# Optimization experiments

Measured on AMD Instinct MI355X. Metric: run time of the kernel, lower is better.

The kernel has to match this reference:

```python
import jax, jax.numpy as jnp
import numpy as np

EPS = 1e-3  # BatchNorm eps from module

def _bn(x, g, b, m, v):
    # torch BatchNorm1d (eval): (x - mean) / sqrt(var + eps) * weight + bias
    return (x - m) * (g / jnp.sqrt(v + EPS)) + b

def setup_inputs() -> dict:
    key = jax.random.key(0)
    ks = jax.random.split(key, 16)
    N, Cin, Cout, S = 1_000_000, 16, 64, 20_000
    inputs = jax.random.normal(ks[0], (N, Cin), dtype=jnp.float32)
    unq_inv = jax.random.randint(ks[1], (N,), 0, S, dtype=jnp.int32)

    def bn_params(k, c):
        k1, k2, k3, k4 = jax.random.split(k, 4)
        return (1.0 + 0.01 * jax.random.normal(k1, (c,), jnp.float32),
                0.01 * jax.random.normal(k2, (c,), jnp.float32),
                0.01 * jax.random.normal(k3, (c,), jnp.float32),
                jax.random.uniform(k4, (c,), jnp.float32, 0.5, 1.5))

    W1 = 0.1 * jax.random.normal(ks[2], (Cin, Cout), jnp.float32)
    g1, b1, m1, v1 = bn_params(ks[3], Cout)
    W2a = 0.1 * jax.random.normal(ks[4], (Cin, 2 * Cout), jnp.float32)
    g2a, b2a, m2a, v2a = bn_params(ks[5], 2 * Cout)
    W2b = 0.1 * jax.random.normal(ks[6], (2 * Cout, Cout), jnp.float32)
    g2b, b2b, m2b, v2b = bn_params(ks[7], Cout)

    return dict(inputs=inputs, unq_inv=unq_inv, num_segments=S,
                W1=W1, g1=g1, b1=b1, m1=m1, v1=v1,
                W2a=W2a, g2a=g2a, b2a=b2a, m2a=m2a, v2a=v2a,
                W2b=W2b, g2b=b2b * 0 + g2b, b2b=b2b, m2b=m2b, v2b=v2b)

def reference(inputs, unq_inv, num_segments,
              W1, g1, b1, m1, v1,
              W2a, g2a, b2a, m2a, v2a,
              W2b, g2b, b2b, m2b, v2b):
    # branch 1: Linear -> BN -> ReLU
    x = jax.nn.relu(_bn(inputs @ W1, g1, b1, m1, v1))            # [N, C]
    # branch 2: Linear -> BN -> ReLU -> Linear -> BN -> ReLU
    h = jax.nn.relu(_bn(inputs @ W2a, g2a, b2a, m2a, v2a))       # [N, 2C]
    x2 = jax.nn.relu(_bn(h @ W2b, g2b, b2b, m2b, v2b))           # [N, C]

    # segment reductions over group ids
    x_max = jax.ops.segment_max(x, unq_inv, num_segments=num_segments)  # [S, C]
    x_max = jnp.maximum(x_max, 0.0)  # empty segments -> 0 (x >= 0 post-ReLU)
    group_sum = jax.ops.segment_sum(x, unq_inv, num_segments=num_segments)  # [S, C]
    max_pool = jnp.max(x2, axis=0)                                # [C], global pool
    max_pool = jnp.broadcast_to(max_pool[None, :], x_max.shape)   # [S, C]

    feat = jnp.concatenate((group_sum, x_max, max_pool), axis=1)  # [S, 3C]
    # channel shuffle with groups=3
    S_, C3 = feat.shape
    feat = feat.reshape(S_, 3, C3 // 3).transpose(0, 2, 1).reshape(S_, C3)
    return feat
```

## Files before the change

### kernel.cpp

```cpp
#include <hip/hip_runtime.h>

#define EPS 1e-3f

#define OFF_T2B    7168
#define OFF_MPP    7232
#define OFF_CNT    11328
#define OFF_OFFS   31344
#define OFF_CUR    51360
#define OFF_INPS   71424

typedef short short8 __attribute__((ext_vector_type(8)));
typedef float f32x4 __attribute__((ext_vector_type(4)));

union U4 { unsigned u[4]; short8 s8; };

__device__ inline unsigned short f2bf(float f) {
    unsigned u = __float_as_uint(f);
    return (unsigned short)((u + 0x7FFFu + ((u >> 16) & 1u)) >> 16);
}

__global__ __launch_bounds__(256) void init_k(
    const float* __restrict__ W1,
    const float* __restrict__ g1, const float* __restrict__ b1,
    const float* __restrict__ m1, const float* __restrict__ v1,
    const float* __restrict__ W2a,
    const float* __restrict__ g2a, const float* __restrict__ b2a,
    const float* __restrict__ m2a, const float* __restrict__ v2a,
    const float* __restrict__ W2b,
    const float* __restrict__ g2b, const float* __restrict__ b2b,
    const float* __restrict__ m2b, const float* __restrict__ v2b,
    unsigned short* __restrict__ wsu, float* __restrict__ wsf,
    const int* __restrict__ unq, int* __restrict__ cnt, int N)
{
    const int t = threadIdx.x;
    if (blockIdx.x == 0) {
        for (int i = t; i < 64 * 32; i += 256) {
            int ch = i >> 5, k = i & 31;
            float s = g1[ch] * rsqrtf(v1[ch] + EPS);
            float val = (k < 16) ? W1[k * 64 + ch] * s
                      : (k == 16 ? b1[ch] - m1[ch] * s : 0.f);
            wsu[i] = f2bf(val);
        }
        for (int i = t; i < 128 * 32; i += 256) {
            int ch = i >> 5, k = i & 31;
            float s = g2a[ch] * rsqrtf(v2a[ch] + EPS);
            float val = (k < 16) ? W2a[k * 128 + ch] * s
                      : (k == 16 ? b2a[ch] - m2a[ch] * s : 0.f);
            wsu[2048 + i] = f2bf(val);
        }
        for (int i = t; i < 64 * 128; i += 256) {
            int ch = i >> 7, k = i & 127;
            float s = g2b[ch] * rsqrtf(v2b[ch] + EPS);
            wsu[2048 + 4096 + i] = f2bf(W2b[k * 64 + ch] * s);
        }
        if (t < 64) {
            float s = g2b[t] * rsqrtf(v2b[t] + EPS);
            wsf[OFF_T2B + t] = b2b[t] - m2b[t] * s;
        }
    } else {
        const int i = (blockIdx.x - 1) * 256 + t;
        if (i < N) atomicAdd(&cnt[unq[i]], 1);
    }
}

__global__ __launch_bounds__(1024) void scan_k(
    const int* __restrict__ cnt, int* __restrict__ offs,
    int* __restrict__ cur, int S)
{
    __shared__ int tot[1024];
    const int t = threadIdx.x;
    const int E = (S + 1023) >> 10;
    const int i0 = t * E;
    int run = 0;
    for (int j = 0; j < E; ++j) {
        const int i = i0 + j;
        run += (i < S) ? cnt[i] : 0;
    }
    tot[t] = run;
    __syncthreads();
    for (int d = 1; d < 1024; d <<= 1) {
        int x = (t >= d) ? tot[t - d] : 0;
        __syncthreads();
        tot[t] += x;
        __syncthreads();
    }
    int base = (t == 0) ? 0 : tot[t - 1];
    for (int j = 0; j < E; ++j) {
        const int i = i0 + j;
        if (i < S) {
            offs[i] = base;
            cur[i]  = base;
            base += cnt[i];
        }
    }
    if (t == 1023) offs[S] = tot[1023];
}

__global__ __launch_bounds__(512, 2) void scatbr2_k(
    const float* __restrict__ inputs,
    const int*   __restrict__ unq,
    int*         __restrict__ cur,
    uint4*       __restrict__ inpS,
    const uint4* __restrict__ wsw,
    const float* __restrict__ wsf,
    float* __restrict__ mpp,
    int N)
{
    __shared__ __align__(16) char w2as[8192];
    __shared__ __align__(16) char w2bs[16384];
    __shared__ float t2bs[64];
    __shared__ float mpb[64];
    __shared__ __align__(16) char scrs[8][4096];

    const int tid = threadIdx.x;
    {
        int u = tid;
        *reinterpret_cast<uint4*>(&w2as[(u * 16) ^ (((u >> 2) & 7) << 4)]) = wsw[256 + u];
        for (int v = tid; v < 1024; v += 512)
            *reinterpret_cast<uint4*>(&w2bs[(v * 16) ^ (((v >> 4) & 7) << 4)]) = wsw[768 + v];
        if (tid < 64) { t2bs[tid] = wsf[OFF_T2B + tid]; mpb[tid] = 0.f; }
    }
    __syncthreads();

    const int wv   = tid >> 6;
    const int lane = tid & 63;
    const int c = lane & 15;
    const int g = lane >> 4;
    const unsigned swz = (unsigned)(lane & 7) << 4;
    char* scr = scrs[wv];

    const long wave_pt0 = (long)blockIdx.x * 512 + (long)wv * 64;
    const long nrem_w = (long)N - wave_pt0;

    f32x4 t2br[4];
    #pragma unroll
    for (int mt = 0; mt < 4; ++mt)
        t2br[mt] = *reinterpret_cast<const f32x4*>(&t2bs[mt * 16 + g * 4]);

    const f32x4 zero4 = {0.f, 0.f, 0.f, 0.f};
    float mp[16];
    #pragma unroll
    for (int j = 0; j < 16; ++j) mp[j] = 0.f;

    #pragma unroll
    for (int ti = 0; ti < 4; ++ti) {
        if ((long)ti * 16 >= nrem_w) break;
        const bool act = (long)(ti * 16 + c) < nrem_w;
        const long pt  = wave_pt0 + ti * 16 + c;

        U4 bf;
        if (g < 2) {
            const long row = act ? pt : (long)(N - 1);
            const float4* p = reinterpret_cast<const float4*>(inputs + row * 16 + g * 8);
            float4 f0 = p[0], f1 = p[1];
            asm("v_cvt_pk_bf16_f32 %0, %1, %2" : "=v"(bf.u[0]) : "v"(f0.x), "v"(f0.y));
            asm("v_cvt_pk_bf16_f32 %0, %1, %2" : "=v"(bf.u[1]) : "v"(f0.z), "v"(f0.w));
            asm("v_cvt_pk_bf16_f32 %0, %1, %2" : "=v"(bf.u[2]) : "v"(f1.x), "v"(f1.y));
            asm("v_cvt_pk_bf16_f32 %0, %1, %2" : "=v"(bf.u[3]) : "v"(f1.z), "v"(f1.w));
            if (!act) { bf.u[0] = 0u; bf.u[1] = 0u; bf.u[2] = 0u; bf.u[3] = 0u; }
        } else {
            bf.u[0] = (g == 2 && act) ? 0x00003F80u : 0u;
            bf.u[1] = 0u; bf.u[2] = 0u; bf.u[3] = 0u;
        }

        int pos = 0;
        if (g == 0 && act) pos = atomicAdd(&cur[unq[pt]], 1);
        pos = __shfl(pos, c, 64);
        if (g < 2 && act)
            inpS[(size_t)pos * 2 + g] = make_uint4(bf.u[0], bf.u[1], bf.u[2], bf.u[3]);

        #pragma unroll
        for (int mt = 0; mt < 8; ++mt) {
            short8 a = *reinterpret_cast<const short8*>(
                &w2as[(unsigned)((mt * 16 + c) * 64 + g * 16) ^ swz]);
            f32x4 hT = __builtin_amdgcn_mfma_f32_16x16x32_bf16(a, bf.s8, zero4, 0, 0, 0);
            float h0 = fmaxf(hT[0], 0.f), h1 = fmaxf(hT[1], 0.f);
            float h2 = fmaxf(hT[2], 0.f), h3 = fmaxf(hT[3], 0.f);
            unsigned lo, hi;
            asm("v_cvt_pk_bf16_f32 %0, %1, %2" : "=v"(lo) : "v"(h0), "v"(h1));
            asm("v_cvt_pk_bf16_f32 %0, %1, %2" : "=v"(hi) : "v"(h2), "v"(h3));
            *reinterpret_cast<uint2*>(
                &scr[(unsigned)(c * 256 + mt * 32 + g * 8) ^ swz]) = make_uint2(lo, hi);
        }

        f32x4 y2t[4];
        #pragma unroll
        for (int mt = 0; mt < 4; ++mt) y2t[mt] = zero4;
        #pragma unroll
        for (int ks = 0; ks < 4; ++ks) {
            short8 hb = *reinterpret_cast<const short8*>(
                &scr[(unsigned)(c * 256 + ks * 64 + g * 16) ^ swz]);
            #pragma unroll
            for (int mt = 0; mt < 4; ++mt) {
                short8 a = *reinterpret_cast<const short8*>(
                    &w2bs[(unsigned)((mt * 16 + c) * 256 + ks * 64 + g * 16) ^ swz]);
                y2t[mt] = __builtin_amdgcn_mfma_f32_16x16x32_bf16(a, hb, y2t[mt], 0, 0, 0);
            }
        }
        #pragma unroll
        for (int mt = 0; mt < 4; ++mt) {
            #pragma unroll
            for (int r = 0; r < 4; ++r) {
                float v = fmaxf(y2t[mt][r] + t2br[mt][r], 0.f);
                if (act) mp[mt * 4 + r] = fmaxf(mp[mt * 4 + r], v);
            }
        }
    }

    #pragma unroll
    for (int j = 0; j < 16; ++j) {
        float x = mp[j];
        x = fmaxf(x, __shfl_xor(x, 1, 64));
        x = fmaxf(x, __shfl_xor(x, 2, 64));
        x = fmaxf(x, __shfl_xor(x, 4, 64));
        x = fmaxf(x, __shfl_xor(x, 8, 64));
        mp[j] = x;
    }
    if (c == 0) {
        #pragma unroll
        for (int mt = 0; mt < 4; ++mt)
            #pragma unroll
            for (int r = 0; r < 4; ++r)
                atomicMax(reinterpret_cast<int*>(&mpb[mt * 16 + g * 4 + r]),
                          __float_as_int(mp[mt * 4 + r]));
    }
    __syncthreads();
    if (tid < 64)
        atomicMax(reinterpret_cast<int*>(mpp + (blockIdx.x & 63) * 64 + tid),
                  __float_as_int(mpb[tid]));
}

__global__ __launch_bounds__(512) void seg1_k(
    const uint4* __restrict__ inpS,
    const int*   __restrict__ offs,
    const uint4* __restrict__ wsw,
    const float* __restrict__ mpp,
    float* __restrict__ out,
    int S, int Npt)
{
    __shared__ __align__(16) char w1s[4096];
    __shared__ float mps[64];
    __shared__ float scr3[8][192];

    const int tid = threadIdx.x;
    if (tid < 256) {
        int u = tid;
        *reinterpret_cast<uint4*>(&w1s[(u * 16) ^ (((u >> 2) & 7) << 4)]) = wsw[u];
    }
    if (tid < 64) {
        float m = 0.f;
        #pragma unroll
        for (int s = 0; s < 64; ++s)
            m = fmaxf(m, mpp[s * 64 + tid]);
        mps[tid] = m;
    }
    __syncthreads();

    const int wv   = tid >> 6;
    const int lane = tid & 63;
    const int seg  = blockIdx.x * 8 + wv;
    if (seg >= S) return;

    const int c = lane & 15;
    const int g = lane >> 4;
    const unsigned swz = (unsigned)(lane & 7) << 4;

    const int start = offs[seg];
    const int end   = offs[seg + 1];

    const f32x4 zero4 = {0.f, 0.f, 0.f, 0.f};
    f32x4 as[4], am[4];
    #pragma unroll
    for (int mt = 0; mt < 4; ++mt) { as[mt] = zero4; am[mt] = zero4; }

    for (int base = start; base < end; base += 64) {
        const int nrem = end - base;
        #pragma unroll
        for (int ti = 0; ti < 4; ++ti) {
            if (ti * 16 >= nrem) break;
            const bool act = (ti * 16 + c) < nrem;

            U4 bf;
            if (g < 2) {
                int row = min(base + ti * 16 + c, Npt - 1);
                uint4 q = inpS[(size_t)row * 2 + g];
                bf.u[0] = act ? q.x : 0u;
                bf.u[1] = act ? q.y : 0u;
                bf.u[2] = act ? q.z : 0u;
                bf.u[3] = act ? q.w : 0u;
            } else {
                bf.u[0] = (g == 2 && act) ? 0x00003F80u : 0u;
                bf.u[1] = 0u; bf.u[2] = 0u; bf.u[3] = 0u;
            }
            #pragma unroll
            for (int mt = 0; mt < 4; ++mt) {
                short8 a = *reinterpret_cast<const short8*>(
                    &w1s[(unsigned)((mt * 16 + c) * 64 + g * 16) ^ swz]);
                f32x4 y1t = __builtin_amdgcn_mfma_f32_16x16x32_bf16(a, bf.s8, zero4, 0, 0, 0);
                #pragma unroll
                for (int r = 0; r < 4; ++r) {
                    float v = fmaxf(y1t[r], 0.f);
                    as[mt][r] += v;
                    am[mt][r]  = fmaxf(am[mt][r], v);
                }
            }
        }
    }

    #pragma unroll
    for (int mt = 0; mt < 4; ++mt) {
        #pragma unroll
        for (int r = 0; r < 4; ++r) {
            float xs = as[mt][r], xm = am[mt][r];
            xs += __shfl_xor(xs, 1, 64);  xm = fmaxf(xm, __shfl_xor(xm, 1, 64));
            xs += __shfl_xor(xs, 2, 64);  xm = fmaxf(xm, __shfl_xor(xm, 2, 64));
            xs += __shfl_xor(xs, 4, 64);  xm = fmaxf(xm, __shfl_xor(xm, 4, 64));
            xs += __shfl_xor(xs, 8, 64);  xm = fmaxf(xm, __shfl_xor(xm, 8, 64));
            as[mt][r] = xs; am[mt][r] = xm;
        }
    }

    float* sr = scr3[wv];
    if (c == 0) {
        #pragma unroll
        for (int mt = 0; mt < 4; ++mt)
            #pragma unroll
            for (int r = 0; r < 4; ++r) {
                const int ch = mt * 16 + g * 4 + r;
                sr[ch * 3 + 0] = as[mt][r];
                sr[ch * 3 + 1] = am[mt][r];
            }
    }
    sr[lane * 3 + 2] = mps[lane];
    __builtin_amdgcn_wave_barrier();
    asm volatile("s_waitcnt lgkmcnt(0)" ::: "memory");
    __builtin_amdgcn_sched_barrier(0);

    float* o = out + (size_t)seg * 192;
    #pragma unroll
    for (int p = 0; p < 3; ++p)
        o[p * 64 + lane] = sr[p * 64 + lane];
}

extern "C" void kernel_launch(void* const* d_in, const int* in_sizes, int n_in,
                              void* d_out, int out_size, void* d_ws, size_t ws_size,
                              hipStream_t stream)
{
    const float* inputs = (const float*)d_in[0];
    const int*   unq    = (const int*)d_in[1];
    const float* W1  = (const float*)d_in[3];
    const float* g1  = (const float*)d_in[4];
    const float* b1  = (const float*)d_in[5];
    const float* m1  = (const float*)d_in[6];
    const float* v1  = (const float*)d_in[7];
    const float* W2a = (const float*)d_in[8];
    const float* g2a = (const float*)d_in[9];
    const float* b2a = (const float*)d_in[10];
    const float* m2a = (const float*)d_in[11];
    const float* v2a = (const float*)d_in[12];
    const float* W2b = (const float*)d_in[13];
    const float* g2b = (const float*)d_in[14];
    const float* b2b = (const float*)d_in[15];
    const float* m2b = (const float*)d_in[16];
    const float* v2b = (const float*)d_in[17];

    float* wsf = (float*)d_ws;
    float* out = (float*)d_out;
    const int N = in_sizes[0] / 16;
    const int S = out_size / 192;

    float* mpp  = wsf + OFF_MPP;
    int*   cnt  = (int*)(wsf + OFF_CNT);
    int*   offs = (int*)(wsf + OFF_OFFS);
    int*   cur  = (int*)(wsf + OFF_CUR);
    uint4* inpS = (uint4*)(wsf + OFF_INPS);

    hipMemsetAsync(mpp, 0, (size_t)(OFF_CNT + 20016 - OFF_MPP) * sizeof(float), stream);

    init_k<<<1 + (N + 255) / 256, 256, 0, stream>>>(
        W1, g1, b1, m1, v1, W2a, g2a, b2a, m2a, v2a, W2b, g2b, b2b, m2b, v2b,
        (unsigned short*)d_ws, wsf, unq, cnt, N);

    scan_k<<<1, 1024, 0, stream>>>(cnt, offs, cur, S);

    scatbr2_k<<<(N + 511) / 512, 512, 0, stream>>>(inputs, unq, cur, inpS,
                                                   (const uint4*)d_ws, wsf, mpp, N);

    seg1_k<<<(S + 7) / 8, 512, 0, stream>>>(inpS, offs, (const uint4*)d_ws,
                                            mpp, out, S, N);
}
```

Baseline: 205.7 us.

## Pre-pack weights in MFMA fragment order, hoist atomics, raise occupancy bounds

Weights are stored in per-lane MFMA fragment order so the A-operand loads become linear, unswizzled LDS reads, and seg1_k keeps the W1 fragments in registers. The scatter atomics are issued once per wave, one per lane, before the tile loop, and each position is fetched by shuffle instead of being done per sub-tile. Launch bounds are raised to 4 blocks per CU, and wave/sched barriers are added to control instruction scheduling. The higher occupancy target may force register spills, and removing the early breaks means partial tiles now do redundant MFMA work.

```diff
diff --git a/kernel.cpp b/kernel.cpp
--- a/kernel.cpp
+++ b/kernel.cpp
@@ -12,7 +12,7 @@
 typedef short short8 __attribute__((ext_vector_type(8)));
 typedef float f32x4 __attribute__((ext_vector_type(4)));
 
-union U4 { unsigned u[4]; short8 s8; };
+union U4 { unsigned u[4]; short8 s8; uint4 u4; };
 
 __device__ inline unsigned short f2bf(float f) {
     unsigned u = __float_as_uint(f);
@@ -34,24 +34,31 @@
 {
     const int t = threadIdx.x;
     if (blockIdx.x == 0) {
-        for (int i = t; i < 64 * 32; i += 256) {
-            int ch = i >> 5, k = i & 31;
+        for (int i = t; i < 2048; i += 256) {
+            int mt = i >> 9, lane = (i >> 3) & 63, j = i & 7;
+            int c = lane & 15, g = lane >> 4;
+            int k = g * 8 + j, ch = mt * 16 + c;
             float s = g1[ch] * rsqrtf(v1[ch] + EPS);
             float val = (k < 16) ? W1[k * 64 + ch] * s
                       : (k == 16 ? b1[ch] - m1[ch] * s : 0.f);
             wsu[i] = f2bf(val);
         }
-        for (int i = t; i < 128 * 32; i += 256) {
-            int ch = i >> 5, k = i & 31;
+        for (int i = t; i < 4096; i += 256) {
+            int mt = i >> 9, lane = (i >> 3) & 63, j = i & 7;
+            int c = lane & 15, g = lane >> 4;
+            int k = g * 8 + j, ch = mt * 16 + c;
             float s = g2a[ch] * rsqrtf(v2a[ch] + EPS);
             float val = (k < 16) ? W2a[k * 128 + ch] * s
                       : (k == 16 ? b2a[ch] - m2a[ch] * s : 0.f);
             wsu[2048 + i] = f2bf(val);
         }
-        for (int i = t; i < 64 * 128; i += 256) {
-            int ch = i >> 7, k = i & 127;
+        for (int i = t; i < 8192; i += 256) {
+            int f = i >> 9, lane = (i >> 3) & 63, j = i & 7;
+            int mt = f >> 2, ks = f & 3;
+            int c = lane & 15, g = lane >> 4;
+            int k = ks * 32 + g * 8 + j, ch = mt * 16 + c;
             float s = g2b[ch] * rsqrtf(v2b[ch] + EPS);
-            wsu[2048 + 4096 + i] = f2bf(W2b[k * 64 + ch] * s);
+            wsu[6144 + i] = f2bf(W2b[k * 64 + ch] * s);
         }
         if (t < 64) {
             float s = g2b[t] * rsqrtf(v2b[t] + EPS);
@@ -96,7 +103,7 @@
     if (t == 1023) offs[S] = tot[1023];
 }
 
-__global__ __launch_bounds__(512, 2) void scatbr2_k(
+__global__ __launch_bounds__(512, 4) void scatbr2_k(
     const float* __restrict__ inputs,
     const int*   __restrict__ unq,
     int*         __restrict__ cur,
@@ -106,18 +113,16 @@
     float* __restrict__ mpp,
     int N)
 {
-    __shared__ __align__(16) char w2as[8192];
-    __shared__ __align__(16) char w2bs[16384];
+    __shared__ __align__(16) char wlds[24576];
     __shared__ float t2bs[64];
     __shared__ float mpb[64];
     __shared__ __align__(16) char scrs[8][4096];
 
     const int tid = threadIdx.x;
     {
-        int u = tid;
-        *reinterpret_cast<uint4*>(&w2as[(u * 16) ^ (((u >> 2) & 7) << 4)]) = wsw[256 + u];
-        for (int v = tid; v < 1024; v += 512)
-            *reinterpret_cast<uint4*>(&w2bs[(v * 16) ^ (((v >> 4) & 7) << 4)]) = wsw[768 + v];
+        #pragma unroll
+        for (int u = 0; u < 3; ++u)
+            reinterpret_cast<uint4*>(wlds)[u * 512 + tid] = wsw[256 + u * 512 + tid];
         if (tid < 64) { t2bs[tid] = wsf[OFF_T2B + tid]; mpb[tid] = 0.f; }
     }
     __syncthreads();
@@ -126,17 +131,22 @@
     const int lane = tid & 63;
     const int c = lane & 15;
     const int g = lane >> 4;
-    const unsigned swz = (unsigned)(lane & 7) << 4;
     char* scr = scrs[wv];
 
     const long wave_pt0 = (long)blockIdx.x * 512 + (long)wv * 64;
     const long nrem_w = (long)N - wave_pt0;
+    if (nrem_w <= 0) return;
 
     f32x4 t2br[4];
     #pragma unroll
     for (int mt = 0; mt < 4; ++mt)
         t2br[mt] = *reinterpret_cast<const f32x4*>(&t2bs[mt * 16 + g * 4]);
 
+    const long ip = wave_pt0 + lane;
+    const bool lane_ok = (ip < (long)N);
+    int pos = 0;
+    if (lane_ok) pos = atomicAdd(&cur[unq[ip]], 1);
+
     const f32x4 zero4 = {0.f, 0.f, 0.f, 0.f};
     float mp[16];
     #pragma unroll
@@ -144,13 +154,11 @@
 
     #pragma unroll
     for (int ti = 0; ti < 4; ++ti) {
-        if ((long)ti * 16 >= nrem_w) break;
         const bool act = (long)(ti * 16 + c) < nrem_w;
-        const long pt  = wave_pt0 + ti * 16 + c;
 
         U4 bf;
         if (g < 2) {
-            const long row = act ? pt : (long)(N - 1);
+            const long row = act ? (wave_pt0 + ti * 16 + c) : (long)(N - 1);
             const float4* p = reinterpret_cast<const float4*>(inputs + row * 16 + g * 8);
             float4 f0 = p[0], f1 = p[1];
             asm("v_cvt_pk_bf16_f32 %0, %1, %2" : "=v"(bf.u[0]) : "v"(f0.x), "v"(f0.y));
@@ -163,16 +171,13 @@
             bf.u[1] = 0u; bf.u[2] = 0u; bf.u[3] = 0u;
         }
 
-        int pos = 0;
-        if (g == 0 && act) pos = atomicAdd(&cur[unq[pt]], 1);
-        pos = __shfl(pos, c, 64);
+        const int posc = __shfl(pos, ti * 16 + c, 64);
         if (g < 2 && act)
-            inpS[(size_t)pos * 2 + g] = make_uint4(bf.u[0], bf.u[1], bf.u[2], bf.u[3]);
+            inpS[(size_t)posc * 2 + g] = bf.u4;
 
         #pragma unroll
         for (int mt = 0; mt < 8; ++mt) {
-            short8 a = *reinterpret_cast<const short8*>(
-                &w2as[(unsigned)((mt * 16 + c) * 64 + g * 16) ^ swz]);
+            short8 a = *reinterpret_cast<const short8*>(&wlds[(mt * 64 + lane) * 16]);
             f32x4 hT = __builtin_amdgcn_mfma_f32_16x16x32_bf16(a, bf.s8, zero4, 0, 0, 0);
             float h0 = fmaxf(hT[0], 0.f), h1 = fmaxf(hT[1], 0.f);
             float h2 = fmaxf(hT[2], 0.f), h3 = fmaxf(hT[3], 0.f);
@@ -180,8 +185,11 @@
             asm("v_cvt_pk_bf16_f32 %0, %1, %2" : "=v"(lo) : "v"(h0), "v"(h1));
             asm("v_cvt_pk_bf16_f32 %0, %1, %2" : "=v"(hi) : "v"(h2), "v"(h3));
             *reinterpret_cast<uint2*>(
-                &scr[(unsigned)(c * 256 + mt * 32 + g * 8) ^ swz]) = make_uint2(lo, hi);
-        }
+                &scr[(unsigned)(c * 256 + mt * 32 + g * 8) ^ ((unsigned)(c & 7) << 4)])
+                = make_uint2(lo, hi);
+        }
+        __builtin_amdgcn_wave_barrier();
+        __builtin_amdgcn_sched_barrier(0);
 
         f32x4 y2t[4];
         #pragma unroll
@@ -189,11 +197,11 @@
         #pragma unroll
         for (int ks = 0; ks < 4; ++ks) {
             short8 hb = *reinterpret_cast<const short8*>(
-                &scr[(unsigned)(c * 256 + ks * 64 + g * 16) ^ swz]);
+                &scr[(unsigned)(c * 256 + ks * 64 + g * 16) ^ ((unsigned)(c & 7) << 4)]);
             #pragma unroll
             for (int mt = 0; mt < 4; ++mt) {
                 short8 a = *reinterpret_cast<const short8*>(
-                    &w2bs[(unsigned)((mt * 16 + c) * 256 + ks * 64 + g * 16) ^ swz]);
+                    &wlds[8192 + ((mt * 4 + ks) * 64 + lane) * 16]);
                 y2t[mt] = __builtin_amdgcn_mfma_f32_16x16x32_bf16(a, hb, y2t[mt], 0, 0, 0);
             }
         }
@@ -205,6 +213,8 @@
                 if (act) mp[mt * 4 + r] = fmaxf(mp[mt * 4 + r], v);
             }
         }
+        __builtin_amdgcn_wave_barrier();
+        __builtin_amdgcn_sched_barrier(0);
     }
 
     #pragma unroll
@@ -230,23 +240,21 @@
                   __float_as_int(mpb[tid]));
 }
 
-__global__ __launch_bounds__(512) void seg1_k(
+__global__ __launch_bounds__(512, 4) void seg1_k(
     const uint4* __restrict__ inpS,
     const int*   __restrict__ offs,
     const uint4* __restrict__ wsw,
     const float* __restrict__ mpp,
     float* __restrict__ out,
-    int S, int Npt)
+    int S)
 {
-    __shared__ __align__(16) char w1s[4096];
+    __shared__ __align__(16) char w1lds[4096];
     __shared__ float mps[64];
     __shared__ float scr3[8][192];
 
     const int tid = threadIdx.x;
-    if (tid < 256) {
-        int u = tid;
-        *reinterpret_cast<uint4*>(&w1s[(u * 16) ^ (((u >> 2) & 7) << 4)]) = wsw[u];
-    }
+    if (tid < 256)
+        reinterpret_cast<uint4*>(w1lds)[tid] = wsw[tid];
     if (tid < 64) {
         float m = 0.f;
         #pragma unroll
@@ -263,7 +271,11 @@
 
     const int c = lane & 15;
     const int g = lane >> 4;
-    const unsigned swz = (unsigned)(lane & 7) << 4;
+
+    short8 w1[4];
+    #pragma unroll
+    for (int mt = 0; mt < 4; ++mt)
+        w1[mt] = *reinterpret_cast<const short8*>(&w1lds[(mt * 64 + lane) * 16]);
 
     const int start = offs[seg];
     const int end   = offs[seg + 1];
@@ -277,12 +289,11 @@
         const int nrem = end - base;
         #pragma unroll
         for (int ti = 0; ti < 4; ++ti) {
-            if (ti * 16 >= nrem) break;
             const bool act = (ti * 16 + c) < nrem;
 
             U4 bf;
             if (g < 2) {
-                int row = min(base + ti * 16 + c, Npt - 1);
+                const int row = min(base + ti * 16 + c, end - 1);
                 uint4 q = inpS[(size_t)row * 2 + g];
                 bf.u[0] = act ? q.x : 0u;
                 bf.u[1] = act ? q.y : 0u;
@@ -294,9 +305,7 @@
             }
             #pragma unroll
             for (int mt = 0; mt < 4; ++mt) {
-                short8 a = *reinterpret_cast<const short8*>(
-                    &w1s[(unsigned)((mt * 16 + c) * 64 + g * 16) ^ swz]);
-                f32x4 y1t = __builtin_amdgcn_mfma_f32_16x16x32_bf16(a, bf.s8, zero4, 0, 0, 0);
+                f32x4 y1t = __builtin_amdgcn_mfma_f32_16x16x32_bf16(w1[mt], bf.s8, zero4, 0, 0, 0);
                 #pragma unroll
                 for (int r = 0; r < 4; ++r) {
                     float v = fmaxf(y1t[r], 0.f);
@@ -387,5 +396,5 @@
                                                    (const uint4*)d_ws, wsf, mpp, N);
 
     seg1_k<<<(S + 7) / 8, 512, 0, stream>>>(inpS, offs, (const uint4*)d_ws,
-                                            mpp, out, S, N);
-}
+                                            mpp, out, S);
+}
```

New measurement: 259.5 us. +26.2%, slower.
